# Kernel tuning notes

Measured on AMD Instinct MI355X. Metric: run time of the kernel, lower is better.

Reference implementation:

```python
import jax, jax.numpy as jnp
import numpy as np

H = 8
DH = 64
MAX_REL = 32
SCALE = DH ** -0.5


def setup_inputs() -> dict:
    key = jax.random.key(0)
    ks = jax.random.split(key, 10)
    B, T, D = 2, 2048, 512
    s = 1.0 / np.sqrt(D)
    return {
        "hidden_states": jax.random.normal(ks[0], (B, T, D), jnp.float32),
        "Wq": jax.random.normal(ks[1], (D, H * DH), jnp.float32) * s,
        "bq": jax.random.normal(ks[2], (H * DH,), jnp.float32) * 0.02,
        "Wk": jax.random.normal(ks[3], (D, H * DH), jnp.float32) * s,
        "bk": jax.random.normal(ks[4], (H * DH,), jnp.float32) * 0.02,
        "Wv": jax.random.normal(ks[5], (D, H * DH), jnp.float32) * s,
        "bv": jax.random.normal(ks[6], (H * DH,), jnp.float32) * 0.02,
        "Wo": jax.random.normal(ks[7], (H * DH, D), jnp.float32) * s,
        "bo": jax.random.normal(ks[8], (D,), jnp.float32) * 0.02,
        "rel_bias": jax.random.normal(ks[9], (H, 2 * MAX_REL + 1), jnp.float32) * 0.02,
    }


def _rel_pos_bias(rel_bias, Tq, Tk):
    # (H, Tq, Tk) additive bias from clamped relative distances
    rel = jnp.arange(Tq)[:, None] - jnp.arange(Tk)[None, :]
    idx = jnp.clip(rel, -MAX_REL, MAX_REL) + MAX_REL
    return rel_bias[:, idx]


def reference(hidden_states, Wq, bq, Wk, bk, Wv, bv, Wo, bo, rel_bias):
    B, T, D = hidden_states.shape
    # projections (enn.Linear == dense linear map in forward math)
    Q = (hidden_states @ Wq + bq).reshape(B, T, H, DH)
    K = (hidden_states @ Wk + bk).reshape(B, T, H, DH)
    V = (hidden_states @ Wv + bv).reshape(B, T, H, DH)
    attn = jnp.einsum("bthd,bkhd->bhtk", Q, K) * SCALE
    attn = attn + _rel_pos_bias(rel_bias, T, T)[None]
    attn = jax.nn.softmax(attn, axis=-1)
    out = jnp.einsum("bhtk,bkhd->bthd", attn, V).reshape(B, T, H * DH)
    return out @ Wo + bo
```

## Files before the change

### kernel.cpp

```cpp
#include <hip/hip_runtime.h>
#include <stdint.h>
#include <math.h>

#define H 8
#define DH 64
#define T 2048
#define D 512
#define B 2
#define BH 16
#define MAXREL 32
#define NREL (2*MAXREL+1)
#define C1 0.18033688f
#define NW (D*D)

typedef _Float16 half_t;
typedef half_t half8 __attribute__((ext_vector_type(8)));
typedef half_t half4 __attribute__((ext_vector_type(4)));
typedef float f32x4 __attribute__((ext_vector_type(4)));
typedef int int4v __attribute__((ext_vector_type(4)));

typedef __attribute__((address_space(3))) unsigned int lds_uint;
typedef const __attribute__((address_space(1))) unsigned int glb_uint;

__device__ __forceinline__ void gl_lds16(const void* g, void* l) {
    __builtin_amdgcn_global_load_lds((glb_uint*)g, (lds_uint*)l, 16, 0, 0);
}
__device__ __forceinline__ f32x4 zero4() { f32x4 z = {0.f,0.f,0.f,0.f}; return z; }
__device__ __forceinline__ int pkrtz(float a, float b) {
    return __builtin_bit_cast(int, __builtin_amdgcn_cvt_pkrtz(a, b));
}

__global__ __launch_bounds__(256) void prep(
    const float* __restrict__ X,
    const float* __restrict__ Wq, const float* __restrict__ Wk,
    const float* __restrict__ Wv, const float* __restrict__ Wo,
    half_t* __restrict__ Xh, half_t* __restrict__ Wts)
{
    __shared__ half_t Ld[64 * 72];
    const int bid = blockIdx.x;
    const int tid = threadIdx.x;
    if (bid < 1024) {
        const int i = (bid * 256 + tid) * 8;
        const float4 a = *(const float4*)(X + i);
        const float4 b = *(const float4*)(X + i + 4);
        half8 o;
        o[0]=(half_t)a.x; o[1]=(half_t)a.y; o[2]=(half_t)a.z; o[3]=(half_t)a.w;
        o[4]=(half_t)b.x; o[5]=(half_t)b.y; o[6]=(half_t)b.z; o[7]=(half_t)b.w;
        *(half8*)(Xh + i) = o;
    } else {
        const int id = bid - 1024;
        const int z = id >> 6;
        const int tile = id & 63;
        const float* __restrict__ W = (z==0)?Wq:(z==1)?Wk:(z==2)?Wv:Wo;
        half_t* __restrict__ out = Wts + (size_t)z * NW;
        const int k0 = (tile >> 3) * 64;
        const int n0 = (tile & 7) * 64;
        const int r = tid >> 2, c16 = (tid & 3) * 16;
        const float* src = W + (size_t)(k0 + r) * D + n0 + c16;
        #pragma unroll
        for (int j = 0; j < 16; ++j) Ld[r * 72 + c16 + j] = (half_t)src[j];
        __syncthreads();
        half_t tmp[16];
        #pragma unroll
        for (int j = 0; j < 16; ++j) tmp[j] = Ld[(c16 + j) * 72 + r];
        half8* dst = (half8*)(out + (size_t)(n0 + r) * D + k0 + c16);
        dst[0] = *(half8*)&tmp[0];
        dst[1] = *(half8*)&tmp[8];
    }
}

__global__ __launch_bounds__(256) void gemm_qkv(
    const half_t* __restrict__ Xh, const half_t* __restrict__ Wts,
    const float* __restrict__ bq, const float* __restrict__ bk,
    const float* __restrict__ bv,
    half_t* __restrict__ Qh, half_t* __restrict__ Kh, half_t* __restrict__ Vth)
{
    __shared__ half_t As[2][64 * 64];
    __shared__ half_t Bs[2][128 * 64];
    const int tid = threadIdx.x, w = tid >> 6, lane = tid & 63;
    const int l15 = lane & 15, quad = lane >> 4;
    const int m0 = blockIdx.x * 64, n0 = blockIdx.y * 128, z = blockIdx.z;
    const half_t* __restrict__ Wt = Wts + (size_t)z * NW;
    const float* __restrict__ bias = (z==0)?bq:(z==1)?bk:bv;

    auto stage = [&](int buf, int k0) {
        #pragma unroll
        for (int s = 0; s < 2; ++s) {
            const int cid = (w * 2 + s) * 64 + lane;
            const int r = cid >> 3, c = (cid & 7) ^ (r & 7);
            gl_lds16(Xh + (size_t)(m0 + r) * D + k0 + c * 8,
                     &As[buf][(w * 2 + s) * 512]);
        }
        #pragma unroll
        for (int s = 0; s < 4; ++s) {
            const int cid = (w * 4 + s) * 64 + lane;
            const int r = cid >> 3, c = (cid & 7) ^ (r & 7);
            gl_lds16(Wt + (size_t)(n0 + r) * D + k0 + c * 8,
                     &Bs[buf][(w * 4 + s) * 512]);
        }
    };

    f32x4 acc[4][2];
    #pragma unroll
    for (int ms = 0; ms < 4; ++ms) { acc[ms][0] = zero4(); acc[ms][1] = zero4(); }

    stage(0, 0);
    __syncthreads();
    for (int it = 0; it < 8; ++it) {
        const int cur = it & 1;
        if (it < 7) stage(cur ^ 1, (it + 1) * 64);
        const int swiz = l15 & 7;
        #pragma unroll
        for (int ks = 0; ks < 2; ++ks) {
            const int c = (ks * 4 + quad) ^ swiz;
            half8 bf[2];
            #pragma unroll
            for (int nt = 0; nt < 2; ++nt)
                bf[nt] = *(const half8*)&Bs[cur][(w * 32 + nt * 16 + l15) * 64 + c * 8];
            #pragma unroll
            for (int ms = 0; ms < 4; ++ms) {
                const half8 af = *(const half8*)&As[cur][(ms * 16 + l15) * 64 + c * 8];
                acc[ms][0] = __builtin_amdgcn_mfma_f32_16x16x32_f16(af, bf[0], acc[ms][0], 0, 0, 0);
                acc[ms][1] = __builtin_amdgcn_mfma_f32_16x16x32_f16(af, bf[1], acc[ms][1], 0, 0, 0);
            }
        }
        __syncthreads();
    }

    float bvv[2];
    #pragma unroll
    for (int nt = 0; nt < 2; ++nt) bvv[nt] = bias[n0 + w * 32 + nt * 16 + l15];

    if (z == 2) {
        #pragma unroll
        for (int ms = 0; ms < 4; ++ms) {
            const int mbase = m0 + ms * 16 + quad * 4;
            const int bb = mbase >> 11, t0 = mbase & 2047;
            #pragma unroll
            for (int nt = 0; nt < 2; ++nt) {
                const int n = n0 + w * 32 + nt * 16 + l15;
                const int hh = n >> 6, d = n & 63;
                half4 pk;
                #pragma unroll
                for (int r = 0; r < 4; ++r) pk[r] = (half_t)(acc[ms][nt][r] + bvv[nt]);
                *(half4*)(Vth + (((size_t)bb * H + hh) * DH + d) * T + t0) = pk;
            }
        }
    } else {
        half_t* __restrict__ dst = (z == 0) ? Qh : Kh;
        #pragma unroll
        for (int ms = 0; ms < 4; ++ms)
            #pragma unroll
            for (int nt = 0; nt < 2; ++nt)
                #pragma unroll
                for (int r = 0; r < 4; ++r) {
                    const int mrow = m0 + ms * 16 + quad * 4 + r;
                    const int n = n0 + w * 32 + nt * 16 + l15;
                    const int bb = mrow >> 11, t = mrow & 2047, hh = n >> 6, d = n & 63;
                    dst[(((size_t)bb * H + hh) * T + t) * DH + d] = (half_t)(acc[ms][nt][r] + bvv[nt]);
                }
    }
}

__global__ __launch_bounds__(256) void attn_fwd(
    const half_t* __restrict__ Qh, const half_t* __restrict__ Kh,
    const half_t* __restrict__ Vth, const float* __restrict__ relb,
    half_t* __restrict__ Onum, half_t* __restrict__ lsum)
{
    __shared__ half_t Kt[2][4096];
    __shared__ half_t Vt[2][4096];
    __shared__ float rb2[NREL];

    const int tid = threadIdx.x, w = tid >> 6, lane = tid & 63;
    const int l15 = lane & 15, quad = lane >> 4;

    const int bid0 = blockIdx.x;
    const int nid = (bid0 & 7) * 128 + (bid0 >> 3);
    const int qb = nid & 31;
    const int bh = (nid >> 5) & 15;
    const int split = nid >> 9;

    const int q0 = qb * 64;
    const int qw = q0 + w * 16;
    const int kb0 = split * 1024;
    const int h = bh & 7;

    if (tid < NREL) rb2[tid] = relb[h * NREL + tid] * 1.44269504f;

    half8 qf[2];
    const half_t* Qbase = Qh + ((size_t)bh * T + qw) * DH;
    #pragma unroll
    for (int ks = 0; ks < 2; ++ks)
        qf[ks] = *(const half8*)(Qbase + l15 * DH + ks * 32 + quad * 8);

    f32x4 of[4];
    #pragma unroll
    for (int nt = 0; nt < 4; ++nt) of[nt] = zero4();
    float lp = 0.f;

    auto stage = [&](int buf, int kb) {
        #pragma unroll
        for (int s = 0; s < 2; ++s) {
            const int cid = (w * 2 + s) * 64 + lane;
            const int r = cid >> 3, cg = (cid & 7) ^ (r & 7);
            gl_lds16(Kh + ((size_t)bh * T + kb + r) * DH + cg * 8,
                     &Kt[buf][(w * 2 + s) * 512]);
            gl_lds16(Vth + ((size_t)bh * DH + r) * T + kb + cg * 8,
                     &Vt[buf][(w * 2 + s) * 512]);
        }
    };

    stage(0, kb0);
    __syncthreads();

    const int qg = qw + l15;
    const int swiz = l15 & 7;

    for (int it = 0; it < 16; ++it) {
        const int cur = it & 1;
        if (it + 1 < 16) stage(cur ^ 1, kb0 + (it + 1) * 64);
        const int kb = kb0 + it * 64;

        f32x4 st[4];
        #pragma unroll
        for (int nt = 0; nt < 4; ++nt) st[nt] = zero4();
        __builtin_amdgcn_s_setprio(1);
        #pragma unroll
        for (int ks = 0; ks < 2; ++ks) {
            const int c = (ks * 4 + quad) ^ swiz;
            #pragma unroll
            for (int nt = 0; nt < 4; ++nt) {
                const half8 kf = *(const half8*)&Kt[cur][(nt * 16 + l15) * 64 + c * 8];
                st[nt] = __builtin_amdgcn_mfma_f32_16x16x32_f16(kf, qf[ks], st[nt], 0, 0, 0);
            }
        }
        __builtin_amdgcn_s_setprio(0);

        int pd[4][2];
        const bool uni_hi = (qw - (kb + 63)) >= MAXREL;
        const bool uni_lo = ((qw + 15) - kb) <= -MAXREL;
        if (uni_hi || uni_lo) {
            const float bu = uni_hi ? rb2[NREL - 1] : rb2[0];
            #pragma unroll
            for (int nt = 0; nt < 4; ++nt) {
                float p[4];
                #pragma unroll
                for (int r = 0; r < 4; ++r) p[r] = exp2f(fmaf(st[nt][r], C1, bu));
                lp += (p[0] + p[1]) + (p[2] + p[3]);
                pd[nt][0] = pkrtz(p[0], p[1]);
                pd[nt][1] = pkrtz(p[2], p[3]);
            }
        } else {
            #pragma unroll
            for (int nt = 0; nt < 4; ++nt) {
                float p[4];
                #pragma unroll
                for (int r = 0; r < 4; ++r) {
                    const int key = kb + nt * 16 + quad * 4 + r;
                    int rel = qg - key;
                    rel = rel < -MAXREL ? -MAXREL : (rel > MAXREL ? MAXREL : rel);
                    p[r] = exp2f(fmaf(st[nt][r], C1, rb2[rel + MAXREL]));
                }
                lp += (p[0] + p[1]) + (p[2] + p[3]);
                pd[nt][0] = pkrtz(p[0], p[1]);
                pd[nt][1] = pkrtz(p[2], p[3]);
            }
        }

        #pragma unroll
        for (int ks = 0; ks < 2; ++ks) {
            int4v bd;
            #pragma unroll
            for (int d = 0; d < 4; ++d) {
                const int src = ((quad & 1) * 2 + (d >> 1)) * 16 + l15;
                const int va = __shfl(pd[2 * ks][d & 1], src);
                const int vb = __shfl(pd[2 * ks + 1][d & 1], src);
                bd[d] = (quad >> 1) ? vb : va;
            }
            const half8 pf = __builtin_bit_cast(half8, bd);
            const int c = (ks * 4 + quad) ^ swiz;
            __builtin_amdgcn_s_setprio(1);
            #pragma unroll
            for (int nt = 0; nt < 4; ++nt) {
                const half8 vf = *(const half8*)&Vt[cur][(nt * 16 + l15) * 64 + c * 8];
                of[nt] = __builtin_amdgcn_mfma_f32_16x16x32_f16(vf, pf, of[nt], 0, 0, 0);
            }
            __builtin_amdgcn_s_setprio(0);
        }
        __syncthreads();
    }

    const size_t qrow = (size_t)(split * BH + bh) * T + qw + l15;
    half_t* obase = Onum + qrow * DH;
    #pragma unroll
    for (int nt = 0; nt < 4; ++nt) {
        half4 pk;
        #pragma unroll
        for (int r = 0; r < 4; ++r) pk[r] = (half_t)(of[nt][r] * 0.015625f);
        *(half4*)(obase + nt * 16 + quad * 4) = pk;
    }
    lp += __shfl_xor(lp, 16);
    lp += __shfl_xor(lp, 32);
    if (quad == 0) lsum[qrow] = (half_t)(lp * 0.015625f);
}

__global__ __launch_bounds__(256) void gemm_out(
    const half_t* __restrict__ Onum, const half_t* __restrict__ lsum,
    const half_t* __restrict__ Wot,
    const float* __restrict__ bo, float* __restrict__ out)
{
    __shared__ half_t As[2][32 * 64];
    __shared__ half_t Bs[2][128 * 64];
    const int tid = threadIdx.x, w = tid >> 6, lane = tid & 63;
    const int l15 = lane & 15, quad = lane >> 4;
    const int m0 = blockIdx.x * 32, n0 = blockIdx.y * 128;

    const int ar = tid >> 3;
    const int ac = (tid & 7) ^ (ar & 7);
    const int rr = m0 + ar;
    const int ab = rr >> 11, at = rr & 2047;

    half8 x0, x1; half_t la, lb;
    auto loadA = [&](int k0) {
        const int bh = ab * H + (k0 >> 6);
        const int d = ac * 8;
        x0 = *(const half8*)(Onum + ((size_t)bh * T + at) * DH + d);
        x1 = *(const half8*)(Onum + ((size_t)(BH + bh) * T + at) * DH + d);
        la = lsum[(size_t)bh * T + at];
        lb = lsum[(size_t)(BH + bh) * T + at];
    };
    auto writeA = [&](int buf) {
        const float inv = 1.0f / ((float)la + (float)lb);
        half8 o;
        #pragma unroll
        for (int j = 0; j < 8; ++j)
            o[j] = (half_t)(((float)x0[j] + (float)x1[j]) * inv);
        *(half8*)&As[buf][tid * 8] = o;
    };

    auto stageB = [&](int buf, int k0) {
        #pragma unroll
        for (int s = 0; s < 4; ++s) {
            const int cid = (w * 4 + s) * 64 + lane;
            const int r = cid >> 3, c = (cid & 7) ^ (r & 7);
            gl_lds16(Wot + (size_t)(n0 + r) * D + k0 + c * 8,
                     &Bs[buf][(w * 4 + s) * 512]);
        }
    };

    f32x4 acc[2][2];
    #pragma unroll
    for (int ms = 0; ms < 2; ++ms) { acc[ms][0] = zero4(); acc[ms][1] = zero4(); }

    loadA(0);
    stageB(0, 0);
    writeA(0);
    __syncthreads();
    for (int it = 0; it < 8; ++it) {
        const int cur = it & 1;
        if (it < 7) { loadA((it + 1) * 64); stageB(cur ^ 1, (it + 1) * 64); }
        const int swiz = l15 & 7;
        #pragma unroll
        for (int ks = 0; ks < 2; ++ks) {
            const int c = (ks * 4 + quad) ^ swiz;
            half8 bf[2];
            #pragma unroll
            for (int nt = 0; nt < 2; ++nt)
                bf[nt] = *(const half8*)&Bs[cur][(w * 32 + nt * 16 + l15) * 64 + c * 8];
            #pragma unroll
            for (int ms = 0; ms < 2; ++ms) {
                const half8 af = *(const half8*)&As[cur][(ms * 16 + l15) * 64 + c * 8];
                acc[ms][0] = __builtin_amdgcn_mfma_f32_16x16x32_f16(af, bf[0], acc[ms][0], 0, 0, 0);
                acc[ms][1] = __builtin_amdgcn_mfma_f32_16x16x32_f16(af, bf[1], acc[ms][1], 0, 0, 0);
            }
        }
        if (it < 7) writeA(cur ^ 1);
        __syncthreads();
    }

    float bvv[2];
    #pragma unroll
    for (int nt = 0; nt < 2; ++nt) bvv[nt] = bo[n0 + w * 32 + nt * 16 + l15];
    #pragma unroll
    for (int ms = 0; ms < 2; ++ms)
        #pragma unroll
        for (int nt = 0; nt < 2; ++nt)
            #pragma unroll
            for (int r = 0; r < 4; ++r) {
                const int mrow = m0 + ms * 16 + quad * 4 + r;
                const int n = n0 + w * 32 + nt * 16 + l15;
                out[(size_t)mrow * D + n] = acc[ms][nt][r] + bvv[nt];
            }
}

extern "C" void kernel_launch(void* const* d_in, const int* in_sizes, int n_in,
                              void* d_out, int out_size, void* d_ws, size_t ws_size,
                              hipStream_t stream)
{
    const float* hs   = (const float*)d_in[0];
    const float* Wq   = (const float*)d_in[1];
    const float* bq   = (const float*)d_in[2];
    const float* Wk   = (const float*)d_in[3];
    const float* bk   = (const float*)d_in[4];
    const float* Wv   = (const float*)d_in[5];
    const float* bv   = (const float*)d_in[6];
    const float* Wo   = (const float*)d_in[7];
    const float* bo   = (const float*)d_in[8];
    const float* relb = (const float*)d_in[9];

    const size_t NX = (size_t)B * T * D;
    half_t* wsh = (half_t*)d_ws;
    half_t* Xh  = wsh;
    half_t* Wts = Xh + NX;
    half_t* Qh  = Wts + 4 * (size_t)NW;
    half_t* Kh  = Qh + NX;
    half_t* Vth = Kh + NX;
    half_t* On  = Vth + NX;
    half_t* Ls  = On + 2 * NX;

    prep    <<<dim3(1280), 256, 0, stream>>>(hs, Wq, Wk, Wv, Wo, Xh, Wts);
    gemm_qkv<<<dim3(64, 4, 3), 256, 0, stream>>>(Xh, Wts, bq, bk, bv, Qh, Kh, Vth);
    attn_fwd<<<dim3(1024), 256, 0, stream>>>(Qh, Kh, Vth, relb, On, Ls);
    gemm_out<<<dim3(128, 4), 256, 0, stream>>>(On, Ls, Wts + 3 * (size_t)NW, bo, (float*)d_out);
}
```

Measured before the change: 139.7 us.

## Switch attention to 32x32x16 MFMA with 128-query blocks

Rewrites the attention kernel to use 32x32x16 MFMA instructions, with each wave handling 32 query rows and each block covering 128 queries. The grid is halved to 512 blocks. Each K/V tile staged in LDS is therefore reused across twice as many queries, and the score-to-operand shuffle drops to one cross-half exchange. The cost is more accumulator registers per thread and fewer blocks, which may lower occupancy and leave CUs underused.

```diff
diff --git a/kernel.cpp b/kernel.cpp
--- a/kernel.cpp
+++ b/kernel.cpp
@@ -17,6 +17,7 @@
 typedef half_t half8 __attribute__((ext_vector_type(8)));
 typedef half_t half4 __attribute__((ext_vector_type(4)));
 typedef float f32x4 __attribute__((ext_vector_type(4)));
+typedef float f32x16 __attribute__((ext_vector_type(16)));
 typedef int int4v __attribute__((ext_vector_type(4)));
 
 typedef __attribute__((address_space(3))) unsigned int lds_uint;
@@ -172,30 +173,32 @@
     __shared__ float rb2[NREL];
 
     const int tid = threadIdx.x, w = tid >> 6, lane = tid & 63;
-    const int l15 = lane & 15, quad = lane >> 4;
+    const int l31 = lane & 31, hi = lane >> 5;
 
     const int bid0 = blockIdx.x;
-    const int nid = (bid0 & 7) * 128 + (bid0 >> 3);
-    const int qb = nid & 31;
-    const int bh = (nid >> 5) & 15;
-    const int split = nid >> 9;
-
-    const int q0 = qb * 64;
-    const int qw = q0 + w * 16;
+    const int nid = (bid0 & 7) * 64 + (bid0 >> 3);
+    const int qb = nid & 15;
+    const int bh = (nid >> 4) & 15;
+    const int split = nid >> 8;
+
+    const int q0 = qb * 128;
+    const int qw = q0 + w * 32;
     const int kb0 = split * 1024;
     const int h = bh & 7;
 
     if (tid < NREL) rb2[tid] = relb[h * NREL + tid] * 1.44269504f;
 
-    half8 qf[2];
+    half8 qf[4];
     const half_t* Qbase = Qh + ((size_t)bh * T + qw) * DH;
     #pragma unroll
-    for (int ks = 0; ks < 2; ++ks)
-        qf[ks] = *(const half8*)(Qbase + l15 * DH + ks * 32 + quad * 8);
-
-    f32x4 of[4];
-    #pragma unroll
-    for (int nt = 0; nt < 4; ++nt) of[nt] = zero4();
+    for (int dblk = 0; dblk < 4; ++dblk)
+        qf[dblk] = *(const half8*)(Qbase + l31 * DH + dblk * 16 + hi * 8);
+
+    f32x16 of[2];
+    #pragma unroll
+    for (int dt = 0; dt < 2; ++dt)
+        #pragma unroll
+        for (int r = 0; r < 16; ++r) of[dt][r] = 0.f;
     float lp = 0.f;
 
     auto stage = [&](int buf, int kb) {
@@ -213,95 +216,104 @@
     stage(0, kb0);
     __syncthreads();
 
-    const int qg = qw + l15;
-    const int swiz = l15 & 7;
+    const int qg = qw + l31;
+    const int sw7 = lane & 7;
 
     for (int it = 0; it < 16; ++it) {
         const int cur = it & 1;
         if (it + 1 < 16) stage(cur ^ 1, kb0 + (it + 1) * 64);
         const int kb = kb0 + it * 64;
 
-        f32x4 st[4];
-        #pragma unroll
-        for (int nt = 0; nt < 4; ++nt) st[nt] = zero4();
+        f32x16 st[2];
+        #pragma unroll
+        for (int mt = 0; mt < 2; ++mt)
+            #pragma unroll
+            for (int r = 0; r < 16; ++r) st[mt][r] = 0.f;
         __builtin_amdgcn_s_setprio(1);
         #pragma unroll
-        for (int ks = 0; ks < 2; ++ks) {
-            const int c = (ks * 4 + quad) ^ swiz;
-            #pragma unroll
-            for (int nt = 0; nt < 4; ++nt) {
-                const half8 kf = *(const half8*)&Kt[cur][(nt * 16 + l15) * 64 + c * 8];
-                st[nt] = __builtin_amdgcn_mfma_f32_16x16x32_f16(kf, qf[ks], st[nt], 0, 0, 0);
+        for (int dblk = 0; dblk < 4; ++dblk) {
+            const int c = (dblk * 2 + hi) ^ sw7;
+            #pragma unroll
+            for (int mt = 0; mt < 2; ++mt) {
+                const half8 kf = *(const half8*)&Kt[cur][(mt * 32 + l31) * 64 + c * 8];
+                st[mt] = __builtin_amdgcn_mfma_f32_32x32x16_f16(kf, qf[dblk], st[mt], 0, 0, 0);
             }
         }
         __builtin_amdgcn_s_setprio(0);
 
-        int pd[4][2];
+        int pk[2][8];
         const bool uni_hi = (qw - (kb + 63)) >= MAXREL;
-        const bool uni_lo = ((qw + 15) - kb) <= -MAXREL;
+        const bool uni_lo = ((qw + 31) - kb) <= -MAXREL;
         if (uni_hi || uni_lo) {
             const float bu = uni_hi ? rb2[NREL - 1] : rb2[0];
             #pragma unroll
-            for (int nt = 0; nt < 4; ++nt) {
-                float p[4];
-                #pragma unroll
-                for (int r = 0; r < 4; ++r) p[r] = exp2f(fmaf(st[nt][r], C1, bu));
-                lp += (p[0] + p[1]) + (p[2] + p[3]);
-                pd[nt][0] = pkrtz(p[0], p[1]);
-                pd[nt][1] = pkrtz(p[2], p[3]);
+            for (int mt = 0; mt < 2; ++mt) {
+                float p[16];
+                #pragma unroll
+                for (int r = 0; r < 16; ++r) p[r] = exp2f(fmaf(st[mt][r], C1, bu));
+                lp += (((p[0]+p[1])+(p[2]+p[3]))+((p[4]+p[5])+(p[6]+p[7])))
+                    + (((p[8]+p[9])+(p[10]+p[11]))+((p[12]+p[13])+(p[14]+p[15])));
+                #pragma unroll
+                for (int i = 0; i < 8; ++i) pk[mt][i] = pkrtz(p[2*i], p[2*i+1]);
             }
         } else {
             #pragma unroll
-            for (int nt = 0; nt < 4; ++nt) {
-                float p[4];
-                #pragma unroll
-                for (int r = 0; r < 4; ++r) {
-                    const int key = kb + nt * 16 + quad * 4 + r;
+            for (int mt = 0; mt < 2; ++mt) {
+                float p[16];
+                #pragma unroll
+                for (int r = 0; r < 16; ++r) {
+                    const int key = kb + mt * 32 + (r & 3) + 8 * (r >> 2) + 4 * hi;
                     int rel = qg - key;
                     rel = rel < -MAXREL ? -MAXREL : (rel > MAXREL ? MAXREL : rel);
-                    p[r] = exp2f(fmaf(st[nt][r], C1, rb2[rel + MAXREL]));
+                    p[r] = exp2f(fmaf(st[mt][r], C1, rb2[rel + MAXREL]));
                 }
-                lp += (p[0] + p[1]) + (p[2] + p[3]);
-                pd[nt][0] = pkrtz(p[0], p[1]);
-                pd[nt][1] = pkrtz(p[2], p[3]);
-            }
-        }
-
-        #pragma unroll
-        for (int ks = 0; ks < 2; ++ks) {
-            int4v bd;
-            #pragma unroll
-            for (int d = 0; d < 4; ++d) {
-                const int src = ((quad & 1) * 2 + (d >> 1)) * 16 + l15;
-                const int va = __shfl(pd[2 * ks][d & 1], src);
-                const int vb = __shfl(pd[2 * ks + 1][d & 1], src);
-                bd[d] = (quad >> 1) ? vb : va;
-            }
-            const half8 pf = __builtin_bit_cast(half8, bd);
-            const int c = (ks * 4 + quad) ^ swiz;
-            __builtin_amdgcn_s_setprio(1);
-            #pragma unroll
-            for (int nt = 0; nt < 4; ++nt) {
-                const half8 vf = *(const half8*)&Vt[cur][(nt * 16 + l15) * 64 + c * 8];
-                of[nt] = __builtin_amdgcn_mfma_f32_16x16x32_f16(vf, pf, of[nt], 0, 0, 0);
-            }
-            __builtin_amdgcn_s_setprio(0);
-        }
+                lp += (((p[0]+p[1])+(p[2]+p[3]))+((p[4]+p[5])+(p[6]+p[7])))
+                    + (((p[8]+p[9])+(p[10]+p[11]))+((p[12]+p[13])+(p[14]+p[15])));
+                #pragma unroll
+                for (int i = 0; i < 8; ++i) pk[mt][i] = pkrtz(p[2*i], p[2*i+1]);
+            }
+        }
+
+        #pragma unroll
+        for (int mt = 0; mt < 2; ++mt)
+            #pragma unroll
+            for (int s2 = 0; s2 < 2; ++s2) {
+                const int base = s2 * 4;
+                const int x1 = hi ? pk[mt][base + 0] : pk[mt][base + 2];
+                const int x2 = hi ? pk[mt][base + 1] : pk[mt][base + 3];
+                const int y1 = __shfl_xor(x1, 32);
+                const int y2 = __shfl_xor(x2, 32);
+                int4v bd;
+                bd[0] = hi ? y1 : pk[mt][base + 0];
+                bd[1] = hi ? y2 : pk[mt][base + 1];
+                bd[2] = hi ? pk[mt][base + 2] : y1;
+                bd[3] = hi ? pk[mt][base + 3] : y2;
+                const half8 pf = __builtin_bit_cast(half8, bd);
+                const int c = ((mt * 2 + s2) * 2 + hi) ^ sw7;
+                __builtin_amdgcn_s_setprio(1);
+                #pragma unroll
+                for (int dt = 0; dt < 2; ++dt) {
+                    const half8 vf = *(const half8*)&Vt[cur][(dt * 32 + l31) * 64 + c * 8];
+                    of[dt] = __builtin_amdgcn_mfma_f32_32x32x16_f16(vf, pf, of[dt], 0, 0, 0);
+                }
+                __builtin_amdgcn_s_setprio(0);
+            }
         __syncthreads();
     }
 
-    const size_t qrow = (size_t)(split * BH + bh) * T + qw + l15;
+    const size_t qrow = (size_t)(split * BH + bh) * T + qw + l31;
     half_t* obase = Onum + qrow * DH;
     #pragma unroll
-    for (int nt = 0; nt < 4; ++nt) {
-        half4 pk;
-        #pragma unroll
-        for (int r = 0; r < 4; ++r) pk[r] = (half_t)(of[nt][r] * 0.015625f);
-        *(half4*)(obase + nt * 16 + quad * 4) = pk;
-    }
-    lp += __shfl_xor(lp, 16);
+    for (int dt = 0; dt < 2; ++dt)
+        #pragma unroll
+        for (int rr = 0; rr < 4; ++rr) {
+            half4 pkv;
+            #pragma unroll
+            for (int j = 0; j < 4; ++j) pkv[j] = (half_t)(of[dt][rr * 4 + j] * 0.015625f);
+            *(half4*)(obase + dt * 32 + rr * 8 + hi * 4) = pkv;
+        }
     lp += __shfl_xor(lp, 32);
-    if (quad == 0) lsum[qrow] = (half_t)(lp * 0.015625f);
+    if (hi == 0) lsum[qrow] = (half_t)(lp * 0.015625f);
 }
 
 __global__ __launch_bounds__(256) void gemm_out(
@@ -420,6 +432,6 @@
 
     prep    <<<dim3(1280), 256, 0, stream>>>(hs, Wq, Wk, Wv, Wo, Xh, Wts);
     gemm_qkv<<<dim3(64, 4, 3), 256, 0, stream>>>(Xh, Wts, bq, bk, bv, Qh, Kh, Vth);
-    attn_fwd<<<dim3(1024), 256, 0, stream>>>(Qh, Kh, Vth, relb, On, Ls);
+    attn_fwd<<<dim3(512), 256, 0, stream>>>(Qh, Kh, Vth, relb, On, Ls);
     gemm_out<<<dim3(128, 4), 256, 0, stream>>>(On, Ls, Wts + 3 * (size_t)NW, bo, (float*)d_out);
 }
```

Result: no change. 141.3 us (+1.1%).
